# Kernel tuning notes

Measured on AMD Instinct MI355X. Metric: run time of the kernel, lower is better.

## Reference

```python
import jax, jax.numpy as jnp
import numpy as np

N_NODES = 100000
N_EDGES = 3200000
F_IN = 14
HIDDEN = 64


def setup_inputs() -> dict:
    key = jax.random.key(0)
    k = jax.random.split(key, 6)
    x = jax.random.normal(k[0], (N_NODES, F_IN), dtype=jnp.float32)
    edge_index = jax.random.randint(k[1], (2, N_EDGES), 0, N_NODES, dtype=jnp.int32)
    # GCNConv weight [F_IN, HIDDEN] + bias, Linear [HIDDEN, 1] + bias
    W1 = jax.random.normal(k[2], (F_IN, HIDDEN), dtype=jnp.float32) / np.sqrt(F_IN)
    b1 = jnp.zeros((HIDDEN,), dtype=jnp.float32)
    W2 = jax.random.normal(k[3], (HIDDEN, 1), dtype=jnp.float32) / np.sqrt(HIDDEN)
    b2 = jnp.zeros((1,), dtype=jnp.float32)
    return {"x": x, "edge_index": edge_index, "W1": W1, "b1": b1, "W2": W2, "b2": b2}


def reference(x, edge_index, W1, b1, W2, b2):
    n = x.shape[0]
    # GCNConv: transform first (F_IN -> HIDDEN), then normalized aggregation
    h = x @ W1  # [N, H]
    # add self-loops (PyG default add_self_loops=True)
    loop = jnp.arange(n, dtype=edge_index.dtype)
    src = jnp.concatenate([edge_index[0], loop])
    dst = jnp.concatenate([edge_index[1], loop])
    # symmetric degree normalization: deg computed on target nodes
    deg = jax.ops.segment_sum(jnp.ones_like(src, dtype=h.dtype), dst, num_segments=n)
    dinv = jnp.where(deg > 0, jax.lax.rsqrt(jnp.maximum(deg, 1e-12)), 0.0)
    norm = dinv[src] * dinv[dst]  # [E+N]
    # gather -> scale -> scatter-add
    msg = h[src] * norm[:, None]  # [E+N, H]
    agg = jax.ops.segment_sum(msg, dst, num_segments=n) + b1  # [N, H]
    # relu; dropout treated as identity (deterministic eval behavior)
    act = jax.nn.relu(agg)
    return act @ W2 + b2  # [N, 1]
```

## Files before the change

kernel.cpp:

```cpp
#include <hip/hip_runtime.h>
#include <hip/hip_fp16.h>

#define F_IN 14
#define HID 64
#define GB 8
#define GSZ 256
#define PAB 256
#define CAPQ 80
#define SB 17
#define SMASK ((1u << SB) - 1)
#define GEC 9216
#define STCAP 12800

__device__ __forceinline__ __half2 u2h(unsigned u) {
    __half2 r; *reinterpret_cast<unsigned*>(&r) = u; return r;
}
__device__ __forceinline__ unsigned h2u(__half2 h) {
    return *reinterpret_cast<unsigned*>(&h);
}

__global__ void __launch_bounds__(512) k_passA(
        const int* __restrict__ src, const int* __restrict__ dst,
        unsigned* __restrict__ queues, int* __restrict__ qcnt,
        int e, int chunk, int ng) {
    __shared__ unsigned stage[STCAP];
    __shared__ int hist[512];
    __shared__ int start[512];
    __shared__ int cur[512];
    int b = blockIdx.x, t = threadIdx.x;
    hist[t] = 0;
    __syncthreads();
    int beg = b * chunk;
    int end = beg + chunk; if (end > e) end = e;

    for (int i = beg + t * 4; i < end; i += 512 * 4) {
        if (i + 4 <= end) {
            int4 d4 = *(const int4*)(dst + i);
            atomicAdd(&hist[d4.x >> GB], 1);
            atomicAdd(&hist[d4.y >> GB], 1);
            atomicAdd(&hist[d4.z >> GB], 1);
            atomicAdd(&hist[d4.w >> GB], 1);
        } else {
            for (int j = 0; i + j < end; ++j) atomicAdd(&hist[dst[i + j] >> GB], 1);
        }
    }
    __syncthreads();

    start[t] = hist[t];
    __syncthreads();
    for (int off = 1; off < 512; off <<= 1) {
        int v = (t >= off) ? start[t - off] : 0;
        __syncthreads();
        start[t] += v;
        __syncthreads();
    }
    int excl = start[t] - hist[t];
    __syncthreads();
    start[t] = excl;
    cur[t] = excl;
    __syncthreads();

    for (int i = beg + t * 4; i < end; i += 512 * 4) {
        if (i + 4 <= end) {
            int4 d4 = *(const int4*)(dst + i);
            int4 s4 = *(const int4*)(src + i);
            int dd[4] = {d4.x, d4.y, d4.z, d4.w};
            int ss[4] = {s4.x, s4.y, s4.z, s4.w};
#pragma unroll
            for (int j = 0; j < 4; ++j) {
                int pos = atomicAdd(&cur[dd[j] >> GB], 1);
                if (pos < STCAP)
                    stage[pos] = ((unsigned)(dd[j] & (GSZ - 1)) << SB) | (unsigned)ss[j];
            }
        } else {
            for (int j = 0; i + j < end; ++j) {
                int d = dst[i + j], s = src[i + j];
                int pos = atomicAdd(&cur[d >> GB], 1);
                if (pos < STCAP)
                    stage[pos] = ((unsigned)(d & (GSZ - 1)) << SB) | (unsigned)s;
            }
        }
    }
    __syncthreads();

    int sg = t >> 3, lane8 = t & 7;
    for (int g = sg; g < ng; g += 64) {
        int c = hist[g]; if (c > CAPQ) c = CAPQ;
        int s0 = start[g];
        unsigned* qd = queues + ((size_t)g * PAB + b) * CAPQ;
        for (int k = lane8; k < c; k += 8) qd[k] = stage[s0 + k];
        if (lane8 == 0) qcnt[g * PAB + b] = c;
    }
}

__global__ void __launch_bounds__(512) k_csr(
        const unsigned* __restrict__ queues, const int* __restrict__ qcnt,
        const float* __restrict__ x, const float* __restrict__ W1,
        int* __restrict__ csr, unsigned* __restrict__ meta, float* __restrict__ dinv,
        __half* __restrict__ hb, int n) {
    __shared__ int csr_s[GEC];
    __shared__ int hist_s[GSZ];
    __shared__ int scan_s[GSZ];
    __shared__ int cur_s[GSZ];
    __shared__ int qlen_s[PAB];
    __shared__ float ws[F_IN * HID];
    __shared__ float xs[GSZ * F_IN];
    int g = blockIdx.x, t = threadIdx.x;
    if (t < GSZ) hist_s[t] = 0;
    if (t < PAB) qlen_s[t] = qcnt[g * PAB + t];
    for (int i = t; i < F_IN * HID; i += 512) ws[i] = W1[i];
    {
        int base = g << GB;
        int nn = n - base; if (nn > GSZ) nn = GSZ;
        int nf2 = (nn * F_IN) >> 1;
        const float2* xv = (const float2*)(x + (size_t)base * F_IN);
        float2* xsv = (float2*)xs;
        for (int i = t; i < nf2; i += 512) xsv[i] = xv[i];
    }
    __syncthreads();

    const uint4* qv = (const uint4*)(queues + (size_t)g * PAB * CAPQ);
    const int NQ4 = PAB * CAPQ / 4;

    for (int i = t; i < NQ4; i += 512) {
        int qid = i / (CAPQ / 4);
        int w0 = (i % (CAPQ / 4)) * 4;
        int len = qlen_s[qid];
        if (w0 >= len) continue;
        uint4 v = qv[i];
        atomicAdd(&hist_s[v.x >> SB], 1);
        if (w0 + 1 < len) atomicAdd(&hist_s[v.y >> SB], 1);
        if (w0 + 2 < len) atomicAdd(&hist_s[v.z >> SB], 1);
        if (w0 + 3 < len) atomicAdd(&hist_s[v.w >> SB], 1);
    }
    __syncthreads();

    if (t < GSZ) scan_s[t] = hist_s[t];
    __syncthreads();
    for (int off = 1; off < GSZ; off <<= 1) {
        int v = (t < GSZ && t >= off) ? scan_s[t - off] : 0;
        __syncthreads();
        if (t < GSZ) scan_s[t] += v;
        __syncthreads();
    }
    if (t < GSZ) {
        int deg = hist_s[t];
        int rb = scan_s[t] - deg;
        cur_s[t] = rb;
        int d = (g << GB) + t;
        if (d < n) {
            dinv[d] = rsqrtf((float)(deg + 1));
            int rbc = rb < GEC ? rb : GEC;
            int degc = deg;
            if (rbc + degc > GEC) degc = GEC - rbc;
            meta[d] = ((unsigned)degc << 14) | (unsigned)rbc;
        }
    }
    __syncthreads();

    {
        int wave = t >> 6, lane = t & 63;
        int base = g << GB;
        for (int k = 0; k < 32; ++k) {
            int ndl = wave + 8 * k;
            int nd = base + ndl;
            if (nd >= n) break;
            float acc = 0.f;
#pragma unroll
            for (int f = 0; f < F_IN; ++f) acc += xs[ndl * F_IN + f] * ws[f * HID + lane];
            float din = rsqrtf((float)(hist_s[ndl] + 1));
            hb[(size_t)nd * HID + lane] = __float2half(acc * din);
        }
    }

    for (int i = t; i < NQ4; i += 512) {
        int qid = i / (CAPQ / 4);
        int w0 = (i % (CAPQ / 4)) * 4;
        int len = qlen_s[qid];
        if (w0 >= len) continue;
        uint4 v = qv[i];
        { int p = atomicAdd(&cur_s[v.x >> SB], 1); if (p < GEC) csr_s[p] = (int)(v.x & SMASK); }
        if (w0 + 1 < len) { int p = atomicAdd(&cur_s[v.y >> SB], 1); if (p < GEC) csr_s[p] = (int)(v.y & SMASK); }
        if (w0 + 2 < len) { int p = atomicAdd(&cur_s[v.z >> SB], 1); if (p < GEC) csr_s[p] = (int)(v.z & SMASK); }
        if (w0 + 3 < len) { int p = atomicAdd(&cur_s[v.w >> SB], 1); if (p < GEC) csr_s[p] = (int)(v.w & SMASK); }
    }
    __syncthreads();

    int total = scan_s[GSZ - 1];
    if (total > GEC) total = GEC;
    uint4* dstp = (uint4*)(csr + (size_t)g * GEC);
    const uint4* srcp = (const uint4*)csr_s;
    int t4 = (total + 3) >> 2;
    for (int i = t; i < t4; i += 512) dstp[i] = srcp[i];
}

__global__ void __launch_bounds__(256) k_aggout(
        const int* __restrict__ csr, const unsigned* __restrict__ meta,
        const __half* __restrict__ hb, const float* __restrict__ dinv,
        const float* __restrict__ b1, const float* __restrict__ W2,
        const float* __restrict__ b2, float* __restrict__ out, int n) {
    int gid = blockIdx.x * blockDim.x + threadIdx.x;
    int node = gid >> 6;
    int lane = threadIdx.x & 63;
    if (node >= n) return;
    unsigned m = meta[node];
    int rb = (int)(m & 0x3FFFu);
    int cnt = (int)(m >> 14);
    const int* sl = csr + (size_t)(node >> GB) * GEC + rb;
    int oct = lane & 7;
    int grp = lane >> 3;
    const char* hbB = (const char*)hb;
    size_t foff = (size_t)oct << 4;

    uint4 sv = *(const uint4*)(hbB + ((size_t)node << 7) + foff);
    float dv = dinv[node];
    float4 b1a = *(const float4*)(b1 + (oct << 3));
    float4 b1b = *(const float4*)(b1 + (oct << 3) + 4);
    float4 w2a = *(const float4*)(W2 + (oct << 3));
    float4 w2b = *(const float4*)(W2 + (oct << 3) + 4);

    bool ok[6];
    int ss[6];
#pragma unroll
    for (int j = 0; j < 6; ++j) {
        int ej = j * 8 + grp;
        ok[j] = ej < cnt;
        ss[j] = sl[ok[j] ? ej : 0];
    }
    uint4 V[6];
#pragma unroll
    for (int j = 0; j < 6; ++j)
        V[j] = *(const uint4*)(hbB + ((size_t)ss[j] << 7) + foff);

    __half2 A0 = u2h(0u), A1 = u2h(0u), A2 = u2h(0u), A3 = u2h(0u);
#pragma unroll
    for (int j = 0; j < 6; ++j) {
        uint4 v = V[j];
        if (!ok[j]) { v.x = 0u; v.y = 0u; v.z = 0u; v.w = 0u; }
        A0 = __hadd2(A0, u2h(v.x)); A1 = __hadd2(A1, u2h(v.y));
        A2 = __hadd2(A2, u2h(v.z)); A3 = __hadd2(A3, u2h(v.w));
    }
    for (int i = 48; i < cnt; i += 8) {
        int e2 = i + grp;
        bool okr = e2 < cnt;
        int s = sl[okr ? e2 : 0];
        uint4 v = *(const uint4*)(hbB + ((size_t)s << 7) + foff);
        if (!okr) { v.x = 0u; v.y = 0u; v.z = 0u; v.w = 0u; }
        A0 = __hadd2(A0, u2h(v.x)); A1 = __hadd2(A1, u2h(v.y));
        A2 = __hadd2(A2, u2h(v.z)); A3 = __hadd2(A3, u2h(v.w));
    }
#define REDH(A) A = __hadd2(A, u2h(__shfl_xor(h2u(A), 8, 64))); \
                A = __hadd2(A, u2h(__shfl_xor(h2u(A), 16, 64))); \
                A = __hadd2(A, u2h(__shfl_xor(h2u(A), 32, 64)))
    REDH(A0); REDH(A1); REDH(A2); REDH(A3);
#undef REDH
    float2 f0 = __half22float2(A0), f1 = __half22float2(A1);
    float2 f2 = __half22float2(A2), f3 = __half22float2(A3);
    float2 s0f = __half22float2(u2h(sv.x)), s1f = __half22float2(u2h(sv.y));
    float2 s2f = __half22float2(u2h(sv.z)), s3f = __half22float2(u2h(sv.w));
    float a0 = f0.x + s0f.x, a1 = f0.y + s0f.y;
    float a2 = f1.x + s1f.x, a3 = f1.y + s1f.y;
    float a4 = f2.x + s2f.x, a5 = f2.y + s2f.y;
    float a6 = f3.x + s3f.x, a7 = f3.y + s3f.y;
    float p;
    p  = fmaxf(a0 * dv + b1a.x, 0.f) * w2a.x;
    p += fmaxf(a1 * dv + b1a.y, 0.f) * w2a.y;
    p += fmaxf(a2 * dv + b1a.z, 0.f) * w2a.z;
    p += fmaxf(a3 * dv + b1a.w, 0.f) * w2a.w;
    p += fmaxf(a4 * dv + b1b.x, 0.f) * w2b.x;
    p += fmaxf(a5 * dv + b1b.y, 0.f) * w2b.y;
    p += fmaxf(a6 * dv + b1b.z, 0.f) * w2b.z;
    p += fmaxf(a7 * dv + b1b.w, 0.f) * w2b.w;
    p += __shfl_xor(p, 1, 64);
    p += __shfl_xor(p, 2, 64);
    p += __shfl_xor(p, 4, 64);
    if (lane == 0) out[node] = p + b2[0];
}

extern "C" void kernel_launch(void* const* d_in, const int* in_sizes, int n_in,
                              void* d_out, int out_size, void* d_ws, size_t ws_size,
                              hipStream_t stream) {
    const float* x  = (const float*)d_in[0];
    const int*   ei = (const int*)d_in[1];
    const float* W1 = (const float*)d_in[2];
    const float* b1 = (const float*)d_in[3];
    const float* W2 = (const float*)d_in[4];
    const float* b2 = (const float*)d_in[5];
    float* out = (float*)d_out;

    int n = in_sizes[0] / F_IN;
    int e = in_sizes[1] / 2;
    const int* src = ei;
    const int* dst = ei + e;

    int ng = (n + GSZ - 1) >> GB;

    unsigned* queues = (unsigned*)d_ws;
    int*      qcnt   = (int*)(queues + (size_t)ng * PAB * CAPQ);
    int*      csr    = qcnt + (size_t)ng * PAB;
    unsigned* meta   = (unsigned*)(csr + (size_t)ng * GEC);
    float*    dinv   = (float*)(meta + n);
    size_t hoff = ((size_t)(dinv + n) - (size_t)d_ws + 15) & ~(size_t)15;
    __half* hb = (__half*)((char*)d_ws + hoff);

    int chunk = (((e + PAB - 1) / PAB) + 3) & ~3;
    k_passA<<<PAB, 512, 0, stream>>>(src, dst, queues, qcnt, e, chunk, ng);
    k_csr<<<ng, 512, 0, stream>>>(queues, qcnt, x, W1, csr, meta, dinv, hb, n);

    long long tot = (long long)n * HID;
    k_aggout<<<(tot + 255) / 256, 256, 0, stream>>>(csr, meta, hb, dinv, b1, W2, b2, out, n);
}
```

Before: 94.65 us.

## Unroll queue scans by two, read x directly, widen gather prefetch to eight

The CSR-build kernel's two queue scans now process two uint4 queue entries per thread per iteration, issuing both global loads before the shared-memory atomics so more loads are in flight. The shared x staging buffer is removed and x rows are read straight from global memory in the node-transform loop, which frees LDS and may raise occupancy. The aggregation kernel's unrolled first gather grows from 6 to 8 rows per lane group (64 edges), covering more nodes without entering the tail loop at the cost of more registers.

```diff
diff --git a/kernel.cpp b/kernel.cpp
--- a/kernel.cpp
+++ b/kernel.cpp
@@ -104,34 +104,41 @@
     __shared__ int cur_s[GSZ];
     __shared__ int qlen_s[PAB];
     __shared__ float ws[F_IN * HID];
-    __shared__ float xs[GSZ * F_IN];
     int g = blockIdx.x, t = threadIdx.x;
     if (t < GSZ) hist_s[t] = 0;
     if (t < PAB) qlen_s[t] = qcnt[g * PAB + t];
     for (int i = t; i < F_IN * HID; i += 512) ws[i] = W1[i];
-    {
-        int base = g << GB;
-        int nn = n - base; if (nn > GSZ) nn = GSZ;
-        int nf2 = (nn * F_IN) >> 1;
-        const float2* xv = (const float2*)(x + (size_t)base * F_IN);
-        float2* xsv = (float2*)xs;
-        for (int i = t; i < nf2; i += 512) xsv[i] = xv[i];
-    }
     __syncthreads();
 
     const uint4* qv = (const uint4*)(queues + (size_t)g * PAB * CAPQ);
     const int NQ4 = PAB * CAPQ / 4;
 
-    for (int i = t; i < NQ4; i += 512) {
-        int qid = i / (CAPQ / 4);
-        int w0 = (i % (CAPQ / 4)) * 4;
-        int len = qlen_s[qid];
-        if (w0 >= len) continue;
-        uint4 v = qv[i];
-        atomicAdd(&hist_s[v.x >> SB], 1);
-        if (w0 + 1 < len) atomicAdd(&hist_s[v.y >> SB], 1);
-        if (w0 + 2 < len) atomicAdd(&hist_s[v.z >> SB], 1);
-        if (w0 + 3 < len) atomicAdd(&hist_s[v.w >> SB], 1);
+    for (int i = t; i < NQ4; i += 1024) {
+        int i2 = i + 512;
+        int qa = i / (CAPQ / 4);
+        int wa = (i % (CAPQ / 4)) * 4;
+        int la = qlen_s[qa];
+        bool aok = wa < la;
+        bool bex = i2 < NQ4;
+        int qb = bex ? i2 / (CAPQ / 4) : 0;
+        int wb = bex ? (i2 % (CAPQ / 4)) * 4 : 0;
+        int lb = bex ? qlen_s[qb] : 0;
+        bool bok = bex && (wb < lb);
+        uint4 va, vb;
+        if (aok) va = qv[i];
+        if (bok) vb = qv[i2];
+        if (aok) {
+            atomicAdd(&hist_s[va.x >> SB], 1);
+            if (wa + 1 < la) atomicAdd(&hist_s[va.y >> SB], 1);
+            if (wa + 2 < la) atomicAdd(&hist_s[va.z >> SB], 1);
+            if (wa + 3 < la) atomicAdd(&hist_s[va.w >> SB], 1);
+        }
+        if (bok) {
+            atomicAdd(&hist_s[vb.x >> SB], 1);
+            if (wb + 1 < lb) atomicAdd(&hist_s[vb.y >> SB], 1);
+            if (wb + 2 < lb) atomicAdd(&hist_s[vb.z >> SB], 1);
+            if (wb + 3 < lb) atomicAdd(&hist_s[vb.w >> SB], 1);
+        }
     }
     __syncthreads();
 
@@ -165,24 +172,41 @@
             int ndl = wave + 8 * k;
             int nd = base + ndl;
             if (nd >= n) break;
+            const float* xr = x + (size_t)nd * F_IN;
             float acc = 0.f;
 #pragma unroll
-            for (int f = 0; f < F_IN; ++f) acc += xs[ndl * F_IN + f] * ws[f * HID + lane];
+            for (int f = 0; f < F_IN; ++f) acc += xr[f] * ws[f * HID + lane];
             float din = rsqrtf((float)(hist_s[ndl] + 1));
             hb[(size_t)nd * HID + lane] = __float2half(acc * din);
         }
     }
 
-    for (int i = t; i < NQ4; i += 512) {
-        int qid = i / (CAPQ / 4);
-        int w0 = (i % (CAPQ / 4)) * 4;
-        int len = qlen_s[qid];
-        if (w0 >= len) continue;
-        uint4 v = qv[i];
-        { int p = atomicAdd(&cur_s[v.x >> SB], 1); if (p < GEC) csr_s[p] = (int)(v.x & SMASK); }
-        if (w0 + 1 < len) { int p = atomicAdd(&cur_s[v.y >> SB], 1); if (p < GEC) csr_s[p] = (int)(v.y & SMASK); }
-        if (w0 + 2 < len) { int p = atomicAdd(&cur_s[v.z >> SB], 1); if (p < GEC) csr_s[p] = (int)(v.z & SMASK); }
-        if (w0 + 3 < len) { int p = atomicAdd(&cur_s[v.w >> SB], 1); if (p < GEC) csr_s[p] = (int)(v.w & SMASK); }
+    for (int i = t; i < NQ4; i += 1024) {
+        int i2 = i + 512;
+        int qa = i / (CAPQ / 4);
+        int wa = (i % (CAPQ / 4)) * 4;
+        int la = qlen_s[qa];
+        bool aok = wa < la;
+        bool bex = i2 < NQ4;
+        int qb = bex ? i2 / (CAPQ / 4) : 0;
+        int wb = bex ? (i2 % (CAPQ / 4)) * 4 : 0;
+        int lb = bex ? qlen_s[qb] : 0;
+        bool bok = bex && (wb < lb);
+        uint4 va, vb;
+        if (aok) va = qv[i];
+        if (bok) vb = qv[i2];
+        if (aok) {
+            { int p = atomicAdd(&cur_s[va.x >> SB], 1); if (p < GEC) csr_s[p] = (int)(va.x & SMASK); }
+            if (wa + 1 < la) { int p = atomicAdd(&cur_s[va.y >> SB], 1); if (p < GEC) csr_s[p] = (int)(va.y & SMASK); }
+            if (wa + 2 < la) { int p = atomicAdd(&cur_s[va.z >> SB], 1); if (p < GEC) csr_s[p] = (int)(va.z & SMASK); }
+            if (wa + 3 < la) { int p = atomicAdd(&cur_s[va.w >> SB], 1); if (p < GEC) csr_s[p] = (int)(va.w & SMASK); }
+        }
+        if (bok) {
+            { int p = atomicAdd(&cur_s[vb.x >> SB], 1); if (p < GEC) csr_s[p] = (int)(vb.x & SMASK); }
+            if (wb + 1 < lb) { int p = atomicAdd(&cur_s[vb.y >> SB], 1); if (p < GEC) csr_s[p] = (int)(vb.y & SMASK); }
+            if (wb + 2 < lb) { int p = atomicAdd(&cur_s[vb.z >> SB], 1); if (p < GEC) csr_s[p] = (int)(vb.z & SMASK); }
+            if (wb + 3 < lb) { int p = atomicAdd(&cur_s[vb.w >> SB], 1); if (p < GEC) csr_s[p] = (int)(vb.w & SMASK); }
+        }
     }
     __syncthreads();
 
@@ -219,28 +243,28 @@
     float4 w2a = *(const float4*)(W2 + (oct << 3));
     float4 w2b = *(const float4*)(W2 + (oct << 3) + 4);
 
-    bool ok[6];
-    int ss[6];
-#pragma unroll
-    for (int j = 0; j < 6; ++j) {
+    bool ok[8];
+    int ss[8];
+#pragma unroll
+    for (int j = 0; j < 8; ++j) {
         int ej = j * 8 + grp;
         ok[j] = ej < cnt;
         ss[j] = sl[ok[j] ? ej : 0];
     }
-    uint4 V[6];
-#pragma unroll
-    for (int j = 0; j < 6; ++j)
+    uint4 V[8];
+#pragma unroll
+    for (int j = 0; j < 8; ++j)
         V[j] = *(const uint4*)(hbB + ((size_t)ss[j] << 7) + foff);
 
     __half2 A0 = u2h(0u), A1 = u2h(0u), A2 = u2h(0u), A3 = u2h(0u);
 #pragma unroll
-    for (int j = 0; j < 6; ++j) {
+    for (int j = 0; j < 8; ++j) {
         uint4 v = V[j];
         if (!ok[j]) { v.x = 0u; v.y = 0u; v.z = 0u; v.w = 0u; }
         A0 = __hadd2(A0, u2h(v.x)); A1 = __hadd2(A1, u2h(v.y));
         A2 = __hadd2(A2, u2h(v.z)); A3 = __hadd2(A3, u2h(v.w));
     }
-    for (int i = 48; i < cnt; i += 8) {
+    for (int i = 64; i < cnt; i += 8) {
         int e2 = i + grp;
         bool okr = e2 < cnt;
         int s = sl[okr ? e2 : 0];
```

Result: slower. 104.7 us (+10.6%).

## Halve node group size and alias CSR storage onto the queue buffer

Applied to the files above, without the earlier changes.

Node groups shrink from 256 to 128 nodes, and per-queue and per-group edge capacities shrink to match. This roughly doubles the number of k_csr blocks, for better spread across compute units. k_passA's shared histograms grow to 1024 bins, and its scan now has each thread handle two bins. The separate CSR array is removed: each k_csr block writes its compacted CSR back over its own queue region, which cuts workspace footprint and write traffic. The risk is that tighter capacities (48 per queue, 4608 per group) could truncate edges on skewed degree distributions.

```diff
diff --git a/kernel.cpp b/kernel.cpp
--- a/kernel.cpp
+++ b/kernel.cpp
@@ -3,14 +3,16 @@
 
 #define F_IN 14
 #define HID 64
-#define GB 8
-#define GSZ 256
+#define GB 7
+#define GSZ 128
 #define PAB 256
-#define CAPQ 80
+#define CAPQ 48
 #define SB 17
 #define SMASK ((1u << SB) - 1)
-#define GEC 9216
+#define GEC 4608
 #define STCAP 12800
+#define NGMAX 1024
+#define CSTR (PAB * CAPQ)
 
 __device__ __forceinline__ __half2 u2h(unsigned u) {
     __half2 r; *reinterpret_cast<unsigned*>(&r) = u; return r;
@@ -24,11 +26,12 @@
         unsigned* __restrict__ queues, int* __restrict__ qcnt,
         int e, int chunk, int ng) {
     __shared__ unsigned stage[STCAP];
-    __shared__ int hist[512];
-    __shared__ int start[512];
-    __shared__ int cur[512];
+    __shared__ int hist[NGMAX];
+    __shared__ int start[NGMAX];
+    __shared__ int cur[NGMAX];
+    __shared__ int tsum[512];
     int b = blockIdx.x, t = threadIdx.x;
-    hist[t] = 0;
+    hist[t] = 0; hist[t + 512] = 0;
     __syncthreads();
     int beg = b * chunk;
     int end = beg + chunk; if (end > e) end = e;
@@ -46,18 +49,18 @@
     }
     __syncthreads();
 
-    start[t] = hist[t];
+    int h0 = hist[2 * t], h1 = hist[2 * t + 1];
+    tsum[t] = h0 + h1;
     __syncthreads();
     for (int off = 1; off < 512; off <<= 1) {
-        int v = (t >= off) ? start[t - off] : 0;
+        int v = (t >= off) ? tsum[t - off] : 0;
         __syncthreads();
-        start[t] += v;
+        tsum[t] += v;
         __syncthreads();
     }
-    int excl = start[t] - hist[t];
-    __syncthreads();
-    start[t] = excl;
-    cur[t] = excl;
+    int bexcl = tsum[t] - (h0 + h1);
+    start[2 * t] = bexcl;       start[2 * t + 1] = bexcl + h0;
+    cur[2 * t] = bexcl;         cur[2 * t + 1] = bexcl + h0;
     __syncthreads();
 
     for (int i = beg + t * 4; i < end; i += 512 * 4) {
@@ -94,9 +97,9 @@
 }
 
 __global__ void __launch_bounds__(512) k_csr(
-        const unsigned* __restrict__ queues, const int* __restrict__ qcnt,
+        unsigned* __restrict__ queues, const int* __restrict__ qcnt,
         const float* __restrict__ x, const float* __restrict__ W1,
-        int* __restrict__ csr, unsigned* __restrict__ meta, float* __restrict__ dinv,
+        unsigned* __restrict__ meta, float* __restrict__ dinv,
         __half* __restrict__ hb, int n) {
     __shared__ int csr_s[GEC];
     __shared__ int hist_s[GSZ];
@@ -111,7 +114,7 @@
     for (int i = t; i < F_IN * HID; i += 512) ws[i] = W1[i];
     {
         int base = g << GB;
-        int nn = n - base; if (nn > GSZ) nn = GSZ;
+        int nn = n - base; if (nn > GSZ) nn = GSZ; if (nn < 0) nn = 0;
         int nf2 = (nn * F_IN) >> 1;
         const float2* xv = (const float2*)(x + (size_t)base * F_IN);
         float2* xsv = (float2*)xs;
@@ -119,8 +122,8 @@
     }
     __syncthreads();
 
-    const uint4* qv = (const uint4*)(queues + (size_t)g * PAB * CAPQ);
-    const int NQ4 = PAB * CAPQ / 4;
+    const uint4* qv = (const uint4*)(queues + (size_t)g * CSTR);
+    const int NQ4 = CSTR / 4;
 
     for (int i = t; i < NQ4; i += 512) {
         int qid = i / (CAPQ / 4);
@@ -161,7 +164,7 @@
     {
         int wave = t >> 6, lane = t & 63;
         int base = g << GB;
-        for (int k = 0; k < 32; ++k) {
+        for (int k = 0; k < GSZ / 8; ++k) {
             int ndl = wave + 8 * k;
             int nd = base + ndl;
             if (nd >= n) break;
@@ -188,7 +191,7 @@
 
     int total = scan_s[GSZ - 1];
     if (total > GEC) total = GEC;
-    uint4* dstp = (uint4*)(csr + (size_t)g * GEC);
+    uint4* dstp = (uint4*)(queues + (size_t)g * CSTR);
     const uint4* srcp = (const uint4*)csr_s;
     int t4 = (total + 3) >> 2;
     for (int i = t; i < t4; i += 512) dstp[i] = srcp[i];
@@ -206,7 +209,7 @@
     unsigned m = meta[node];
     int rb = (int)(m & 0x3FFFu);
     int cnt = (int)(m >> 14);
-    const int* sl = csr + (size_t)(node >> GB) * GEC + rb;
+    const int* sl = csr + (size_t)(node >> GB) * CSTR + rb;
     int oct = lane & 7;
     int grp = lane >> 3;
     const char* hbB = (const char*)hb;
@@ -296,17 +299,16 @@
     int ng = (n + GSZ - 1) >> GB;
 
     unsigned* queues = (unsigned*)d_ws;
-    int*      qcnt   = (int*)(queues + (size_t)ng * PAB * CAPQ);
-    int*      csr    = qcnt + (size_t)ng * PAB;
-    unsigned* meta   = (unsigned*)(csr + (size_t)ng * GEC);
+    int*      qcnt   = (int*)(queues + (size_t)ng * CSTR);
+    unsigned* meta   = (unsigned*)(qcnt + (size_t)ng * PAB);
     float*    dinv   = (float*)(meta + n);
     size_t hoff = ((size_t)(dinv + n) - (size_t)d_ws + 15) & ~(size_t)15;
     __half* hb = (__half*)((char*)d_ws + hoff);
 
     int chunk = (((e + PAB - 1) / PAB) + 3) & ~3;
     k_passA<<<PAB, 512, 0, stream>>>(src, dst, queues, qcnt, e, chunk, ng);
-    k_csr<<<ng, 512, 0, stream>>>(queues, qcnt, x, W1, csr, meta, dinv, hb, n);
+    k_csr<<<ng, 512, 0, stream>>>(queues, qcnt, x, W1, meta, dinv, hb, n);
 
     long long tot = (long long)n * HID;
-    k_aggout<<<(tot + 255) / 256, 256, 0, stream>>>(csr, meta, hb, dinv, b1, W2, b2, out, n);
-}
+    k_aggout<<<(tot + 255) / 256, 256, 0, stream>>>((const int*)queues, meta, hb, dinv, b1, W2, b2, out, n);
+}
```

Result: no change. 92.95 us (median of 2 runs) (-1.8%).
